# Performance work log

Measured on AMD Instinct MI355X. Metric: run time of the kernel, lower is better.

## Reference

```python
import jax, jax.numpy as jnp
import numpy as np

D = 85  # label-distribution length -> selects A3 branch

def _build_A(d):
    if d == 5:
        base = jnp.arange(5)
        return 1.0 - jnp.abs(base[:, None] - base[None, :]) / 5.0
    if d == 10:
        base = jnp.arange(10)
        return 1.0 - jnp.abs(base[:, None] - base[None, :]) / 10.0
    base = jnp.arange(85)
    return (1.0 - jnp.abs(base[:, None] - base[None, :]) / 85.0).astype(jnp.float32)

def setup_inputs() -> dict:
    key = jax.random.key(0)
    k1, k2 = jax.random.split(key)
    B = 262144
    inp = jax.random.normal(k1, (B, D), dtype=jnp.float32)
    tgt = jax.random.uniform(k2, (B, D), dtype=jnp.float32)
    return {"input": inp, "target": tgt}

def reference(input, target):
    A = _build_A(input.shape[1]).astype(input.dtype)
    diff = jnp.abs(input - target)            # [B, d]
    # per-row quadratic form diff_i^T A diff_i, summed over batch
    q = jnp.einsum('bi,ij,bj->b', diff, A, diff)
    return 0.1 * q.sum()
```

## Files before the change

### kernel.cpp

```cpp
#include <hip/hip_runtime.h>
#include <hip/hip_bf16.h>


#define QFD_D 85
#define ROWS_PER_BLOCK 64
#define THREADS 256

__global__ __launch_bounds__(THREADS, 7) void qfd_kernel(
    const float* __restrict__ in, const float* __restrict__ tgt,
    float* __restrict__ partial) {
    __shared__ float diff[ROWS_PER_BLOCK * QFD_D];
    __shared__ float wsum[THREADS / 64];

    const int tid = threadIdx.x;
    const int E = ROWS_PER_BLOCK * QFD_D;
    const int base = blockIdx.x * E;

    const float4* in4 = reinterpret_cast<const float4*>(in + base);
    const float4* tg4 = reinterpret_cast<const float4*>(tgt + base);
    float4* df4 = reinterpret_cast<float4*>(diff);

    float4 a[5], b[5];
    #pragma unroll
    for (int j = 0; j < 5; ++j) {
        a[j] = in4[tid + j * THREADS];
        b[j] = tg4[tid + j * THREADS];
    }
    float4 at, bt;
    if (tid < 80) {
        at = in4[1280 + tid];
        bt = tg4[1280 + tid];
    }
    #pragma unroll
    for (int j = 0; j < 5; ++j) {
        float4 r;
        r.x = fabsf(a[j].x - b[j].x);
        r.y = fabsf(a[j].y - b[j].y);
        r.z = fabsf(a[j].z - b[j].z);
        r.w = fabsf(a[j].w - b[j].w);
        df4[tid + j * THREADS] = r;
    }
    if (tid < 80) {
        float4 r;
        r.x = fabsf(at.x - bt.x);
        r.y = fabsf(at.y - bt.y);
        r.z = fabsf(at.z - bt.z);
        r.w = fabsf(at.w - bt.w);
        df4[1280 + tid] = r;
    }
    __syncthreads();

    float q = 0.0f;
    if (tid < ROWS_PER_BLOCK) {
        const float* d = &diff[tid * QFD_D];
        float L = 0.0f, sumL = 0.0f, sumL2 = 0.0f;
        #pragma unroll 4
        for (int k = 0; k < QFD_D - 1; ++k) {
            L += d[k];
            sumL += L;
            sumL2 = fmaf(L, L, sumL2);
        }
        const float S = L + d[QFD_D - 1];
        q = fmaf(S, S, -(2.0f / 85.0f) * (S * sumL - sumL2));
    }

    #pragma unroll
    for (int off = 32; off > 0; off >>= 1)
        q += __shfl_down(q, off, 64);
    if ((tid & 63) == 0) wsum[tid >> 6] = q;
    __syncthreads();
    if (tid == 0) {
        float s = 0.0f;
        #pragma unroll
        for (int w = 0; w < THREADS / 64; ++w) s += wsum[w];
        partial[blockIdx.x] = s;
    }
}

__global__ __launch_bounds__(THREADS) void qfd_reduce_kernel(
    const float* __restrict__ partial, float* __restrict__ out, int n) {
    __shared__ float wsum[THREADS / 64];
    const int tid = threadIdx.x;
    float s = 0.0f;
    for (int i = tid; i < n; i += THREADS) s += partial[i];
    #pragma unroll
    for (int off = 32; off > 0; off >>= 1)
        s += __shfl_down(s, off, 64);
    if ((tid & 63) == 0) wsum[tid >> 6] = s;
    __syncthreads();
    if (tid == 0) {
        float t = 0.0f;
        #pragma unroll
        for (int w = 0; w < THREADS / 64; ++w) t += wsum[w];
        out[0] = 0.1f * t;
    }
}

extern "C" void kernel_launch(void* const* d_in, const int* in_sizes, int n_in,
                              void* d_out, int out_size, void* d_ws, size_t ws_size,
                              hipStream_t stream) {
    const float* in  = (const float*)d_in[0];
    const float* tgt = (const float*)d_in[1];
    float* out = (float*)d_out;
    float* partial = (float*)d_ws;

    const int B = in_sizes[0] / QFD_D;
    const int grid = B / ROWS_PER_BLOCK;

    qfd_kernel<<<grid, THREADS, 0, stream>>>(in, tgt, partial);
    qfd_reduce_kernel<<<1, THREADS, 0, stream>>>(partial, out, grid);
}
```

Baseline: 193.4 us.

## Split each row's prefix-sum scan across four lanes and combine with shuffles

The per-row prefix-sum quadratic form was computed serially by only 64 of 256 threads. Now four lanes share each row: each scans a segment of about 21 elements, and the segment partial sums are combined into the full sumL and sumL2 with wave shuffles. This shortens the serial dependency chain and keeps all threads busy after the shared-memory stage. It costs extra shuffle instructions and changes the float summation order, and the occupancy hint on launch bounds is removed, which may change register allocation.

After: 193.8 us. Within noise of the previous version (+0.2%).

```diff
diff --git a/kernel.cpp b/kernel.cpp
--- a/kernel.cpp
+++ b/kernel.cpp
@@ -6,7 +6,7 @@
 #define ROWS_PER_BLOCK 64
 #define THREADS 256
 
-__global__ __launch_bounds__(THREADS, 7) void qfd_kernel(
+__global__ __launch_bounds__(THREADS) void qfd_kernel(
     const float* __restrict__ in, const float* __restrict__ tgt,
     float* __restrict__ partial) {
     __shared__ float diff[ROWS_PER_BLOCK * QFD_D];
@@ -50,24 +50,50 @@
     }
     __syncthreads();
 
-    float q = 0.0f;
-    if (tid < ROWS_PER_BLOCK) {
-        const float* d = &diff[tid * QFD_D];
-        float L = 0.0f, sumL = 0.0f, sumL2 = 0.0f;
-        #pragma unroll 4
-        for (int k = 0; k < QFD_D - 1; ++k) {
-            L += d[k];
-            sumL += L;
-            sumL2 = fmaf(L, L, sumL2);
-        }
-        const float S = L + d[QFD_D - 1];
-        q = fmaf(S, S, -(2.0f / 85.0f) * (S * sumL - sumL2));
+    const int q   = tid & 3;
+    const int row = tid >> 2;
+    const int off = 21 * q + (q != 0);
+    const float* dp = &diff[row * QFD_D + off];
+
+    float l = 0.0f, a1 = 0.0f, b2 = 0.0f;
+    #pragma unroll
+    for (int j = 0; j < 21; ++j) {
+        float v = dp[j];
+        l += v;
+        a1 += l;
+        b2 = fmaf(l, l, b2);
+    }
+    if (q == 0) {
+        float v = dp[21];
+        l += v;
+        a1 += l;
+        b2 = fmaf(l, l, b2);
     }
 
+    const int lane = tid & 63;
+    const int qb   = lane & 60;
+    float s0 = __shfl(l, qb + 0, 64);
+    float s1 = __shfl(l, qb + 1, 64);
+    float s2 = __shfl(l, qb + 2, 64);
+    float s3 = __shfl(l, qb + 3, 64);
+    float S  = (s0 + s1) + (s2 + s3);
+    float P  = (q > 0 ? s0 : 0.0f) + (q > 1 ? s1 : 0.0f) + (q > 2 ? s2 : 0.0f);
+    float len = (q == 0) ? 22.0f : 21.0f;
+    float c1 = fmaf(len, P, a1);
+    float c2 = fmaf(len * P, P, fmaf(2.0f * P, a1, b2));
+    float c1s = __shfl(c1, qb + 0, 64) + __shfl(c1, qb + 1, 64)
+              + __shfl(c1, qb + 2, 64) + __shfl(c1, qb + 3, 64);
+    float c2s = __shfl(c2, qb + 0, 64) + __shfl(c2, qb + 1, 64)
+              + __shfl(c2, qb + 2, 64) + __shfl(c2, qb + 3, 64);
+    float sumL  = c1s - S;
+    float sumL2 = c2s - S * S;
+    float qrow  = fmaf(S, S, -(2.0f / 85.0f) * (S * sumL - sumL2));
+    float val   = (q == 0) ? qrow : 0.0f;
+
     #pragma unroll
-    for (int off = 32; off > 0; off >>= 1)
-        q += __shfl_down(q, off, 64);
-    if ((tid & 63) == 0) wsum[tid >> 6] = q;
+    for (int m = 32; m > 0; m >>= 1)
+        val += __shfl_xor(val, m, 64);
+    if (lane == 0) wsum[tid >> 6] = val;
     __syncthreads();
     if (tid == 0) {
         float s = 0.0f;
@@ -84,8 +110,8 @@
     float s = 0.0f;
     for (int i = tid; i < n; i += THREADS) s += partial[i];
     #pragma unroll
-    for (int off = 32; off > 0; off >>= 1)
-        s += __shfl_down(s, off, 64);
+    for (int m = 32; m > 0; m >>= 1)
+        s += __shfl_xor(s, m, 64);
     if ((tid & 63) == 0) wsum[tid >> 6] = s;
     __syncthreads();
     if (tid == 0) {
```
